# Optimization experiments

Measured on AMD Instinct MI355X. Metric: run time of the kernel, lower is better.

The kernel has to match this reference:

```python
import jax, jax.numpy as jnp
import numpy as np

B, F, E, U = 16384, 1024, 8, 512
EH1, EH2 = 1024, 1024
TH1, TH2 = 512, 256
T = 4


def setup_inputs() -> dict:
    key = jax.random.key(0)
    ks = jax.random.split(key, 16)
    s = lambda k, shape: jax.random.normal(k, shape, dtype=jnp.float32) * 0.02
    return {
        "x": jax.random.normal(ks[0], (B, F), dtype=jnp.float32),
        # stacked expert MLP params [E, ...]
        "We1": s(ks[1], (E, F, EH1)), "be1": s(ks[2], (E, EH1)),
        "We2": s(ks[3], (E, EH1, EH2)), "be2": s(ks[4], (E, EH2)),
        "We3": s(ks[5], (E, EH2, U)), "be3": s(ks[6], (E, U)),
        # per-task gates [T, F, E]
        "Wg": jax.random.normal(ks[7], (T, F, E), dtype=jnp.float32),
        # stacked tower params [T, ...]
        "Wt1": s(ks[8], (T, U, TH1)), "bt1": s(ks[9], (T, TH1)),
        "Wt2": s(ks[10], (T, TH1, TH2)), "bt2": s(ks[11], (T, TH2)),
        "Wt3": s(ks[12], (T, TH2, 1)), "bt3": s(ks[13], (T, 1)),
    }


def reference(x, We1, be1, We2, be2, We3, be3, Wg, Wt1, bt1, Wt2, bt2, Wt3, bt3):
    relu = jax.nn.relu
    # experts: all E small MLPs batched as one grouped GEMM chain -> [E, B, U]
    h = relu(jnp.einsum('bf,efh->ebh', x, We1) + be1[:, None, :])
    h = relu(jnp.einsum('ebh,ehk->ebk', h, We2) + be2[:, None, :])
    expert_out = jnp.einsum('ebk,eku->ebu', h, We3) + be3[:, None, :]
    # per-task gates: softmax over expert axis -> [T, B, E]
    gates = jax.nn.softmax(jnp.einsum('bf,tfe->tbe', x, Wg), axis=-1)
    # gate-weighted combine over experts -> [T, B, U]
    ti = jnp.einsum('tbe,ebu->tbu', gates, expert_out)
    # per-task towers -> [T, B, 1]
    g = relu(jnp.einsum('tbu,tuh->tbh', ti, Wt1) + bt1[:, None, :])
    g = relu(jnp.einsum('tbh,thk->tbk', g, Wt2) + bt2[:, None, :])
    out = jnp.einsum('tbk,tko->tbo', g, Wt3) + bt3[:, None, :]
    return out  # [T, B, 1], equivalent to list of per-task [B, 1] outputs
```

## Files before the change

kernel.cpp:

```cpp
#include <hip/hip_runtime.h>
#include <hip/hip_bf16.h>
#include <cstdint>

#define B_ 16384
#define F_ 1024
#define E_ 8
#define U_ 512
#define EH1_ 1024
#define EH2_ 1024
#define TH1_ 512
#define TH2_ 256
#define T_ 4

typedef __attribute__((ext_vector_type(4))) float f32x4;
typedef __attribute__((ext_vector_type(8))) short bf16x8;
typedef __attribute__((ext_vector_type(4))) short s16x4;

__device__ __forceinline__ short f2bf(float f) {
  union { float f; unsigned u; } v; v.f = f;
  unsigned r = v.u + 0x7fffu + ((v.u >> 16) & 1u);
  return (short)(r >> 16);
}
__device__ __forceinline__ float bf2f(short s) {
  union { unsigned u; float f; } v; v.u = ((unsigned)(unsigned short)s) << 16;
  return v.f;
}

__device__ __forceinline__ void gload16(const void* g, void* l) {
  __builtin_amdgcn_global_load_lds(
      (const __attribute__((address_space(1))) void*)g,
      (__attribute__((address_space(3))) void*)l, 16, 0, 0);
}

__global__ __launch_bounds__(256) void trans_conv(const float* __restrict__ W,
                                                  short* __restrict__ Wt, int K, int N) {
  __shared__ float tile[32][33];
  const int e = blockIdx.z;
  const int k0 = blockIdx.x * 32, n0 = blockIdx.y * 32;
  const float* We = W + (size_t)e * K * N;
  short* Wte = Wt + (size_t)e * N * K;
  const int tx = threadIdx.x, ty = threadIdx.y;
#pragma unroll
  for (int r = 0; r < 32; r += 8)
    tile[ty + r][tx] = We[(size_t)(k0 + ty + r) * N + (n0 + tx)];
  __syncthreads();
#pragma unroll
  for (int r = 0; r < 32; r += 8)
    Wte[(size_t)(n0 + ty + r) * K + (k0 + tx)] = f2bf(tile[tx][ty + r]);
}

__global__ __launch_bounds__(256) void trans_wg(const float* __restrict__ Wg,
                                                short* __restrict__ Wp,
                                                short* __restrict__ Wr) {
  int idx = blockIdx.x * 256 + threadIdx.x;
  int p = idx >> 10, f = idx & 1023;
  int t = p >> 3, e = p & 7;
  float w = Wg[((size_t)t * F_ + f) * E_ + e];
  short wb = f2bf(w);
  Wp[idx] = wb;
  Wr[idx] = f2bf(w - bf2f(wb));
}

__global__ __launch_bounds__(256) void prep_gates(const float* __restrict__ x,
                                                  short* __restrict__ xb,
                                                  const short* __restrict__ Wp,
                                                  const short* __restrict__ Wr,
                                                  float* __restrict__ gates) {
  const int wid = threadIdx.x >> 6, lane = threadIdx.x & 63;
  const int m0 = blockIdx.x * 64 + wid * 16;
  const int fr = lane & 15, kg = (lane >> 4) * 8;
  f32x4 acc[2];
#pragma unroll
  for (int j = 0; j < 2; j++)
#pragma unroll
    for (int r = 0; r < 4; r++) acc[j][r] = 0.f;

  const float* xrow = x + (size_t)(m0 + fr) * F_ + kg;
  short* xbrow = xb + (size_t)(m0 + fr) * F_ + kg;
  const short* Wp0 = Wp + (size_t)fr * F_ + kg;
  const short* Wp1 = Wp + (size_t)(16 + fr) * F_ + kg;
  const short* Wr0 = Wr + (size_t)fr * F_ + kg;
  const short* Wr1 = Wr + (size_t)(16 + fr) * F_ + kg;

  for (int k0 = 0; k0 < F_; k0 += 32) {
    float4 v0 = *(const float4*)(xrow + k0);
    float4 v1 = *(const float4*)(xrow + k0 + 4);
    float v[8] = {v0.x, v0.y, v0.z, v0.w, v1.x, v1.y, v1.z, v1.w};
    bf16x8 ab, ar;
#pragma unroll
    for (int j = 0; j < 8; j++) {
      short s = f2bf(v[j]);
      ab[j] = s;
      ar[j] = f2bf(v[j] - bf2f(s));
    }
    *(bf16x8*)(xbrow + k0) = ab;
    bf16x8 wp0 = *(const bf16x8*)(Wp0 + k0);
    bf16x8 wp1 = *(const bf16x8*)(Wp1 + k0);
    bf16x8 wr0 = *(const bf16x8*)(Wr0 + k0);
    bf16x8 wr1 = *(const bf16x8*)(Wr1 + k0);
    acc[0] = __builtin_amdgcn_mfma_f32_16x16x32_bf16(ab, wp0, acc[0], 0, 0, 0);
    acc[1] = __builtin_amdgcn_mfma_f32_16x16x32_bf16(ab, wp1, acc[1], 0, 0, 0);
    acc[0] = __builtin_amdgcn_mfma_f32_16x16x32_bf16(ab, wr0, acc[0], 0, 0, 0);
    acc[1] = __builtin_amdgcn_mfma_f32_16x16x32_bf16(ab, wr1, acc[1], 0, 0, 0);
    acc[0] = __builtin_amdgcn_mfma_f32_16x16x32_bf16(ar, wp0, acc[0], 0, 0, 0);
    acc[1] = __builtin_amdgcn_mfma_f32_16x16x32_bf16(ar, wp1, acc[1], 0, 0, 0);
  }

  const int cc = lane & 15;
#pragma unroll
  for (int j = 0; j < 2; ++j) {
    const int t = j * 2 + (cc >> 3), e = cc & 7;
#pragma unroll
    for (int r = 0; r < 4; ++r) {
      float s = acc[j][r];
      float mx = s;
      mx = fmaxf(mx, __shfl_xor(mx, 1, 64));
      mx = fmaxf(mx, __shfl_xor(mx, 2, 64));
      mx = fmaxf(mx, __shfl_xor(mx, 4, 64));
      float ex = __expf(s - mx);
      float sm = ex;
      sm += __shfl_xor(sm, 1, 64);
      sm += __shfl_xor(sm, 2, 64);
      sm += __shfl_xor(sm, 4, 64);
      const int b = m0 + (lane >> 4) * 4 + r;
      gates[((size_t)t * B_ + b) * E_ + e] = ex / sm;
    }
  }
}

template <int RELU>
__global__ __launch_bounds__(256, 2) void gemm_bt(const short* __restrict__ A0, size_t sA,
                                                  const short* __restrict__ B0, size_t sB,
                                                  const float* __restrict__ bias0, size_t sBias,
                                                  short* __restrict__ C0, size_t sC,
                                                  int M, int N, int K) {
  const int z = blockIdx.z;
  const short* A = A0 + (size_t)z * sA;
  const short* Bt = B0 + (size_t)z * sB;
  const float* bias = bias0 + (size_t)z * sBias;
  short* C = C0 + (size_t)z * sC;

  __shared__ short As[128 * 64];
  __shared__ short Bs[128 * 64];
  const int tid = threadIdx.x;
  const int wid = tid >> 6;
  const int lane = tid & 63;
  const int m0 = blockIdx.x * 128;
  const int n0 = blockIdx.y * 128;
  const int wm = (wid >> 1) * 64;
  const int wn = (wid & 1) * 64;

  f32x4 acc[4][4];
#pragma unroll
  for (int i = 0; i < 4; i++)
#pragma unroll
    for (int j = 0; j < 4; j++)
#pragma unroll
      for (int r = 0; r < 4; r++) acc[i][j][r] = 0.f;

  const int srow8 = lane >> 3;
  const int scolb = (((lane & 7) ^ srow8) << 4);
  const short* aS = A + (size_t)(m0 + wid * 8 + srow8) * K + (scolb >> 1);
  const short* bS = Bt + (size_t)(n0 + wid * 8 + srow8) * K + (scolb >> 1);
  char* Adst = (char*)As + wid * 1024;
  char* Bdst = (char*)Bs + wid * 1024;

  const int fr = lane & 15;
  const int g = lane >> 4;
  const int swzR = (fr & 7) << 4;
  const char* Ard = (const char*)As + (wm + fr) * 128;
  const char* Brd = (const char*)Bs + (wn + fr) * 128;

  for (int k0 = 0; k0 < K; k0 += 64) {
#pragma unroll
    for (int c = 0; c < 4; ++c) {
      gload16(aS + (size_t)c * 32 * K + k0, Adst + c * 4096);
      gload16(bS + (size_t)c * 32 * K + k0, Bdst + c * 4096);
    }
    __syncthreads();
    {
      const int ca = (g * 16) ^ swzR;
      bf16x8 af[4], bfv[4];
#pragma unroll
      for (int i = 0; i < 4; i++) af[i] = *(const bf16x8*)(Ard + i * 2048 + ca);
#pragma unroll
      for (int j = 0; j < 4; j++) bfv[j] = *(const bf16x8*)(Brd + j * 2048 + ca);
      __builtin_amdgcn_s_setprio(1);
#pragma unroll
      for (int i = 0; i < 4; i++)
#pragma unroll
        for (int j = 0; j < 4; j++)
          acc[i][j] = __builtin_amdgcn_mfma_f32_16x16x32_bf16(af[i], bfv[j], acc[i][j], 0, 0, 0);
      __builtin_amdgcn_s_setprio(0);
    }
    {
      const int ca = (64 + g * 16) ^ swzR;
      bf16x8 af[4], bfv[4];
#pragma unroll
      for (int i = 0; i < 4; i++) af[i] = *(const bf16x8*)(Ard + i * 2048 + ca);
#pragma unroll
      for (int j = 0; j < 4; j++) bfv[j] = *(const bf16x8*)(Brd + j * 2048 + ca);
      __builtin_amdgcn_s_setprio(1);
#pragma unroll
      for (int i = 0; i < 4; i++)
#pragma unroll
        for (int j = 0; j < 4; j++)
          acc[i][j] = __builtin_amdgcn_mfma_f32_16x16x32_bf16(af[i], bfv[j], acc[i][j], 0, 0, 0);
      __builtin_amdgcn_s_setprio(0);
    }
    __syncthreads();
  }

  const int cr4 = (lane >> 4) * 4;
  const int cc = lane & 15;
#pragma unroll
  for (int j = 0; j < 4; j++) {
    const int col = n0 + wn + j * 16 + cc;
    const float bv = bias[col];
#pragma unroll
    for (int i = 0; i < 4; i++) {
      const int row = m0 + wm + i * 16 + cr4;
#pragma unroll
      for (int r = 0; r < 4; r++) {
        float v = acc[i][j][r] + bv;
        if (RELU) v = fmaxf(v, 0.f);
        C[(size_t)(row + r) * N + col] = f2bf(v);
      }
    }
  }
}

__global__ __launch_bounds__(256) void combine_kernel(const short* __restrict__ EO,
                                                      const float* __restrict__ gates,
                                                      short* __restrict__ ti,
                                                      int Bc, int b0) {
  const int idx = blockIdx.x * 256 + threadIdx.x;
  const int lb = idx >> 6;
  const int uc = (idx & 63) * 8;
  float acc[T_][8];
#pragma unroll
  for (int t = 0; t < T_; t++)
#pragma unroll
    for (int j = 0; j < 8; j++) acc[t][j] = 0.f;
#pragma unroll
  for (int e = 0; e < E_; e++) {
    bf16x8 v = *(const bf16x8*)&EO[((size_t)e * Bc + lb) * U_ + uc];
    float f[8];
#pragma unroll
    for (int j = 0; j < 8; j++) f[j] = bf2f(v[j]);
#pragma unroll
    for (int t = 0; t < T_; t++) {
      const float g = gates[((size_t)t * B_ + b0 + lb) * E_ + e];
#pragma unroll
      for (int j = 0; j < 8; j++) acc[t][j] += g * f[j];
    }
  }
#pragma unroll
  for (int t = 0; t < T_; t++) {
    bf16x8 o;
#pragma unroll
    for (int j = 0; j < 8; j++) o[j] = f2bf(acc[t][j]);
    *(bf16x8*)&ti[((size_t)t * Bc + lb) * U_ + uc] = o;
  }
}

__global__ __launch_bounds__(256) void tower3_kernel(const short* __restrict__ G2,
                                                     const float* __restrict__ Wt3,
                                                     const float* __restrict__ bt3,
                                                     float* __restrict__ out,
                                                     int bcShift, int b0) {
  const int wid = threadIdx.x >> 6, lane = threadIdx.x & 63;
  const int rowl = blockIdx.x * 4 + wid;
  const int t = rowl >> bcShift;
  const int lb = rowl & ((1 << bcShift) - 1);
  const short* g = G2 + (size_t)rowl * TH2_;
  s16x4 gv = *(const s16x4*)(g + lane * 4);
  float4 wv = *(const float4*)(Wt3 + t * TH2_ + lane * 4);
  float s = bf2f(gv[0]) * wv.x + bf2f(gv[1]) * wv.y + bf2f(gv[2]) * wv.z + bf2f(gv[3]) * wv.w;
#pragma unroll
  for (int off = 32; off; off >>= 1) s += __shfl_xor(s, off, 64);
  if (lane == 0) out[(size_t)t * B_ + b0 + lb] = s + bt3[t];
}

extern "C" void kernel_launch(void* const* d_in, const int* in_sizes, int n_in,
                              void* d_out, int out_size, void* d_ws, size_t ws_size,
                              hipStream_t stream) {
  const float* x   = (const float*)d_in[0];
  const float* We1 = (const float*)d_in[1];
  const float* be1 = (const float*)d_in[2];
  const float* We2 = (const float*)d_in[3];
  const float* be2 = (const float*)d_in[4];
  const float* We3 = (const float*)d_in[5];
  const float* be3 = (const float*)d_in[6];
  const float* Wg  = (const float*)d_in[7];
  const float* Wt1 = (const float*)d_in[8];
  const float* bt1 = (const float*)d_in[9];
  const float* Wt2 = (const float*)d_in[10];
  const float* bt2 = (const float*)d_in[11];
  const float* Wt3 = (const float*)d_in[12];
  const float* bt3 = (const float*)d_in[13];
  float* out = (float*)d_out;
  (void)in_sizes; (void)n_in; (void)out_size;

  char* ws = (char*)d_ws;
  size_t off = 0;
  auto alloc = [&](size_t bytes) {
    char* p = ws + off;
    off += (bytes + 255) & ~(size_t)255;
    return p;
  };
  short* We1b  = (short*)alloc((size_t)E_ * F_ * EH1_ * 2);
  short* We2b  = (short*)alloc((size_t)E_ * EH1_ * EH2_ * 2);
  short* We3b  = (short*)alloc((size_t)E_ * EH2_ * U_ * 2);
  short* Wt1b  = (short*)alloc((size_t)T_ * U_ * TH1_ * 2);
  short* Wt2b  = (short*)alloc((size_t)T_ * TH1_ * TH2_ * 2);
  short* Wgp   = (short*)alloc((size_t)32 * F_ * 2);
  short* Wgr   = (short*)alloc((size_t)32 * F_ * 2);
  float* gates = (float*)alloc((size_t)T_ * B_ * E_ * 4);
  short* xb    = (short*)alloc((size_t)B_ * F_ * 2);
  const size_t persist = off;

  int Bc = 16384;
  while (Bc > 256 && persist + (size_t)Bc * 32768 + 65536 > ws_size) Bc >>= 1;
  const int bcShift = __builtin_ctz((unsigned)Bc);

  short* h1 = (short*)alloc((size_t)E_ * Bc * EH1_ * 2);
  short* h2 = (short*)alloc((size_t)E_ * Bc * EH2_ * 2);
  short* EO = h1;
  short* ti = h2;
  short* G1 = h2 + (size_t)Bc * 2048;
  short* G2 = h2 + (size_t)Bc * 4096;

  dim3 tb(32, 8);
  trans_conv<<<dim3(F_ / 32, EH1_ / 32, E_), tb, 0, stream>>>(We1, We1b, F_, EH1_);
  trans_conv<<<dim3(EH1_ / 32, EH2_ / 32, E_), tb, 0, stream>>>(We2, We2b, EH1_, EH2_);
  trans_conv<<<dim3(EH2_ / 32, U_ / 32, E_), tb, 0, stream>>>(We3, We3b, EH2_, U_);
  trans_conv<<<dim3(U_ / 32, TH1_ / 32, T_), tb, 0, stream>>>(Wt1, Wt1b, U_, TH1_);
  trans_conv<<<dim3(TH1_ / 32, TH2_ / 32, T_), tb, 0, stream>>>(Wt2, Wt2b, TH1_, TH2_);
  trans_wg<<<(32 * F_) / 256, 256, 0, stream>>>(Wg, Wgp, Wgr);

  prep_gates<<<B_ / 64, 256, 0, stream>>>(x, xb, Wgp, Wgr, gates);

  for (int b0 = 0; b0 < B_; b0 += Bc) {
    const short* xc = xb + (size_t)b0 * F_;
    gemm_bt<1><<<dim3(Bc / 128, EH1_ / 128, E_), 256, 0, stream>>>(
        xc, 0, We1b, (size_t)F_ * EH1_, be1, EH1_, h1, (size_t)Bc * EH1_, Bc, EH1_, F_);
    gemm_bt<1><<<dim3(Bc / 128, EH2_ / 128, E_), 256, 0, stream>>>(
        h1, (size_t)Bc * EH1_, We2b, (size_t)EH1_ * EH2_, be2, EH2_, h2, (size_t)Bc * EH2_,
        Bc, EH2_, EH1_);
    gemm_bt<0><<<dim3(Bc / 128, U_ / 128, E_), 256, 0, stream>>>(
        h2, (size_t)Bc * EH2_, We3b, (size_t)EH2_ * U_, be3, U_, EO, (size_t)Bc * U_,
        Bc, U_, EH2_);
    combine_kernel<<<(Bc * 64) / 256, 256, 0, stream>>>(EO, gates, ti, Bc, b0);
    gemm_bt<1><<<dim3(Bc / 128, TH1_ / 128, T_), 256, 0, stream>>>(
        ti, (size_t)Bc * U_, Wt1b, (size_t)U_ * TH1_, bt1, TH1_, G1, (size_t)Bc * TH1_,
        Bc, TH1_, U_);
    gemm_bt<1><<<dim3(Bc / 128, TH2_ / 128, T_), 256, 0, stream>>>(
        G1, (size_t)Bc * TH1_, Wt2b, (size_t)TH1_ * TH2_, bt2, TH2_, G2, (size_t)Bc * TH2_,
        Bc, TH2_, TH1_);
    tower3_kernel<<<T_ * Bc / 4, 256, 0, stream>>>(G2, Wt3, bt3, out, bcShift, b0);
  }
}
```

Baseline: 955.9 us.

## Fuse tower layer 2 and 3 GEMMs and run towers once over full batch

After: 949.0 us. No clear change (-0.7%).

```diff
diff --git a/kernel.cpp b/kernel.cpp
--- a/kernel.cpp
+++ b/kernel.cpp
@@ -14,7 +14,6 @@
 
 typedef __attribute__((ext_vector_type(4))) float f32x4;
 typedef __attribute__((ext_vector_type(8))) short bf16x8;
-typedef __attribute__((ext_vector_type(4))) short s16x4;
 
 __device__ __forceinline__ short f2bf(float f) {
   union { float f; unsigned u; } v; v.f = f;
@@ -233,7 +232,7 @@
 __global__ __launch_bounds__(256) void combine_kernel(const short* __restrict__ EO,
                                                       const float* __restrict__ gates,
                                                       short* __restrict__ ti,
-                                                      int Bc, int b0) {
+                                                      int Bc, int b0, int tiStride, int tiOff) {
   const int idx = blockIdx.x * 256 + threadIdx.x;
   const int lb = idx >> 6;
   const int uc = (idx & 63) * 8;
@@ -260,26 +259,103 @@
     bf16x8 o;
 #pragma unroll
     for (int j = 0; j < 8; j++) o[j] = f2bf(acc[t][j]);
-    *(bf16x8*)&ti[((size_t)t * Bc + lb) * U_ + uc] = o;
-  }
-}
-
-__global__ __launch_bounds__(256) void tower3_kernel(const short* __restrict__ G2,
-                                                     const float* __restrict__ Wt3,
-                                                     const float* __restrict__ bt3,
-                                                     float* __restrict__ out,
-                                                     int bcShift, int b0) {
-  const int wid = threadIdx.x >> 6, lane = threadIdx.x & 63;
-  const int rowl = blockIdx.x * 4 + wid;
-  const int t = rowl >> bcShift;
-  const int lb = rowl & ((1 << bcShift) - 1);
-  const short* g = G2 + (size_t)rowl * TH2_;
-  s16x4 gv = *(const s16x4*)(g + lane * 4);
-  float4 wv = *(const float4*)(Wt3 + t * TH2_ + lane * 4);
-  float s = bf2f(gv[0]) * wv.x + bf2f(gv[1]) * wv.y + bf2f(gv[2]) * wv.z + bf2f(gv[3]) * wv.w;
-#pragma unroll
-  for (int off = 32; off; off >>= 1) s += __shfl_xor(s, off, 64);
-  if (lane == 0) out[(size_t)t * B_ + b0 + lb] = s + bt3[t];
+    *(bf16x8*)&ti[((size_t)t * tiStride + tiOff + lb) * U_ + uc] = o;
+  }
+}
+
+__global__ __launch_bounds__(512, 1) void wt23(const short* __restrict__ G1, size_t sG1,
+                                               const short* __restrict__ W2,
+                                               const float* __restrict__ b2,
+                                               const float* __restrict__ w3,
+                                               const float* __restrict__ b3,
+                                               float* __restrict__ out, int b0) {
+  const int t = blockIdx.z;
+  const short* A = G1 + (size_t)t * sG1;
+  const short* Bt = W2 + (size_t)t * TH1_ * TH2_;
+
+  __shared__ short As[128 * 64];
+  __shared__ short Bs[256 * 64];
+  __shared__ float ps[4][128];
+  const int tid = threadIdx.x, wid = tid >> 6, lane = tid & 63;
+  const int m0 = blockIdx.x * 128;
+  const int wm = (wid >> 2) * 64, wn = (wid & 3) * 64;
+
+  f32x4 acc[4][4];
+#pragma unroll
+  for (int i = 0; i < 4; i++)
+#pragma unroll
+    for (int j = 0; j < 4; j++)
+#pragma unroll
+      for (int r = 0; r < 4; r++) acc[i][j][r] = 0.f;
+
+  const int trow = tid >> 3;
+  const int scolb = (((tid & 7) ^ (trow & 7)) << 4);
+  const short* aS = A + (size_t)(m0 + trow) * TH1_ + (scolb >> 1);
+  const short* bS = Bt + (size_t)trow * TH1_ + (scolb >> 1);
+  char* Adst = (char*)As + wid * 1024;
+  char* Bdst = (char*)Bs + wid * 1024;
+
+  const int fr = lane & 15, g = lane >> 4;
+  const int swzR = (fr & 7) << 4;
+  const char* Ard = (const char*)As + (wm + fr) * 128;
+  const char* Brd = (const char*)Bs + (wn + fr) * 128;
+
+  for (int k0 = 0; k0 < TH1_; k0 += 64) {
+#pragma unroll
+    for (int c = 0; c < 2; ++c)
+      gload16(aS + (size_t)c * 64 * TH1_ + k0, Adst + c * 8192);
+#pragma unroll
+    for (int c = 0; c < 4; ++c)
+      gload16(bS + (size_t)c * 64 * TH1_ + k0, Bdst + c * 8192);
+    __syncthreads();
+#pragma unroll
+    for (int ks = 0; ks < 2; ++ks) {
+      const int ca = (ks * 64 + g * 16) ^ swzR;
+      bf16x8 af[4], bfv[4];
+#pragma unroll
+      for (int i = 0; i < 4; i++) af[i] = *(const bf16x8*)(Ard + i * 2048 + ca);
+#pragma unroll
+      for (int j = 0; j < 4; j++) bfv[j] = *(const bf16x8*)(Brd + j * 2048 + ca);
+      __builtin_amdgcn_s_setprio(1);
+#pragma unroll
+      for (int i = 0; i < 4; i++)
+#pragma unroll
+        for (int j = 0; j < 4; j++)
+          acc[i][j] = __builtin_amdgcn_mfma_f32_16x16x32_bf16(af[i], bfv[j], acc[i][j], 0, 0, 0);
+      __builtin_amdgcn_s_setprio(0);
+    }
+    __syncthreads();
+  }
+
+  const int cc = lane & 15, cr4 = (lane >> 4) * 4;
+  float w3v[4], b2v[4];
+#pragma unroll
+  for (int j = 0; j < 4; ++j) {
+    const int col = wn + j * 16 + cc;
+    w3v[j] = w3[t * TH2_ + col];
+    b2v[j] = b2[t * TH2_ + col];
+  }
+#pragma unroll
+  for (int i = 0; i < 4; ++i)
+#pragma unroll
+    for (int r = 0; r < 4; ++r) {
+      float p = 0.f;
+#pragma unroll
+      for (int j = 0; j < 4; ++j) {
+        float v = fmaxf(acc[i][j][r] + b2v[j], 0.f);
+        p += v * w3v[j];
+      }
+      p += __shfl_xor(p, 1, 64);
+      p += __shfl_xor(p, 2, 64);
+      p += __shfl_xor(p, 4, 64);
+      p += __shfl_xor(p, 8, 64);
+      if (cc == 0) ps[wid & 3][wm + i * 16 + cr4 + r] = p;
+    }
+  __syncthreads();
+  if (tid < 128) {
+    float s = ps[0][tid] + ps[1][tid] + ps[2][tid] + ps[3][tid] + b3[t];
+    out[(size_t)t * B_ + b0 + m0 + tid] = s;
+  }
 }
 
 extern "C" void kernel_launch(void* const* d_in, const int* in_sizes, int n_in,
@@ -320,16 +396,25 @@
   short* xb    = (short*)alloc((size_t)B_ * F_ * 2);
   const size_t persist = off;
 
-  int Bc = 16384;
-  while (Bc > 256 && persist + (size_t)Bc * 32768 + 65536 > ws_size) Bc >>= 1;
+  const size_t tiBytes = ((size_t)T_ * B_ * U_ * 2 + 255) & ~(size_t)255;
+  int Bc = 0;
+  bool full = false;
+  for (int bc = 16384; bc >= 4096; bc >>= 1) {
+    if (persist + tiBytes + (size_t)bc * 32768 + 65536 <= ws_size) { Bc = bc; full = true; break; }
+  }
+  if (!full) {
+    Bc = 16384;
+    while (Bc > 256 && persist + (size_t)Bc * 32768 + 65536 > ws_size) Bc >>= 1;
+  }
   const int bcShift = __builtin_ctz((unsigned)Bc);
-
+  (void)bcShift;
+
+  short* tiFull = full ? (short*)alloc((size_t)T_ * B_ * U_ * 2) : nullptr;
   short* h1 = (short*)alloc((size_t)E_ * Bc * EH1_ * 2);
   short* h2 = (short*)alloc((size_t)E_ * Bc * EH2_ * 2);
   short* EO = h1;
-  short* ti = h2;
-  short* G1 = h2 + (size_t)Bc * 2048;
-  short* G2 = h2 + (size_t)Bc * 4096;
+  short* tiC = h2;
+  short* G1C = h2 + (size_t)Bc * 2048;
 
   dim3 tb(32, 8);
   trans_conv<<<dim3(F_ / 32, EH1_ / 32, E_), tb, 0, stream>>>(We1, We1b, F_, EH1_);
@@ -351,13 +436,24 @@
     gemm_bt<0><<<dim3(Bc / 128, U_ / 128, E_), 256, 0, stream>>>(
         h2, (size_t)Bc * EH2_, We3b, (size_t)EH2_ * U_, be3, U_, EO, (size_t)Bc * U_,
         Bc, U_, EH2_);
-    combine_kernel<<<(Bc * 64) / 256, 256, 0, stream>>>(EO, gates, ti, Bc, b0);
-    gemm_bt<1><<<dim3(Bc / 128, TH1_ / 128, T_), 256, 0, stream>>>(
-        ti, (size_t)Bc * U_, Wt1b, (size_t)U_ * TH1_, bt1, TH1_, G1, (size_t)Bc * TH1_,
-        Bc, TH1_, U_);
-    gemm_bt<1><<<dim3(Bc / 128, TH2_ / 128, T_), 256, 0, stream>>>(
-        G1, (size_t)Bc * TH1_, Wt2b, (size_t)TH1_ * TH2_, bt2, TH2_, G2, (size_t)Bc * TH2_,
-        Bc, TH2_, TH1_);
-    tower3_kernel<<<T_ * Bc / 4, 256, 0, stream>>>(G2, Wt3, bt3, out, bcShift, b0);
-  }
-}
+    if (full) {
+      combine_kernel<<<(Bc * 64) / 256, 256, 0, stream>>>(EO, gates, tiFull, Bc, b0, B_, b0);
+    } else {
+      combine_kernel<<<(Bc * 64) / 256, 256, 0, stream>>>(EO, gates, tiC, Bc, b0, Bc, 0);
+      gemm_bt<1><<<dim3(Bc / 128, TH1_ / 128, T_), 256, 0, stream>>>(
+          tiC, (size_t)Bc * U_, Wt1b, (size_t)U_ * TH1_, bt1, TH1_, G1C, (size_t)Bc * TH1_,
+          Bc, TH1_, U_);
+      wt23<<<dim3(Bc / 128, 1, T_), 512, 0, stream>>>(
+          G1C, (size_t)Bc * TH1_, Wt2b, bt2, Wt3, bt3, out, b0);
+    }
+  }
+
+  if (full) {
+    short* G1 = h1;
+    gemm_bt<1><<<dim3(B_ / 128, TH1_ / 128, T_), 256, 0, stream>>>(
+        tiFull, (size_t)B_ * U_, Wt1b, (size_t)U_ * TH1_, bt1, TH1_,
+        G1, (size_t)B_ * TH1_, B_, TH1_, U_);
+    wt23<<<dim3(B_ / 128, 1, T_), 512, 0, stream>>>(
+        G1, (size_t)B_ * TH1_, Wt2b, bt2, Wt3, bt3, out, 0);
+  }
+}
```
